# Optimization experiments

Measured on AMD Instinct MI355X. Metric: run time of the kernel, lower is better.

## Reference

```python
import jax, jax.numpy as jnp
import numpy as np

B, P, C = 4, 12000, 64
H, W = 512, 512


def setup_inputs() -> dict:
    key = jax.random.key(0)
    k1, k2 = jax.random.split(key)
    pillar_features = jax.random.normal(k1, (B, P, C), dtype=jnp.float32)
    coords = jax.random.randint(k2, (B, P, 4), 0, 512, dtype=jnp.int32)
    return {"pillar_features": pillar_features, "coords": coords}


def reference(pillar_features, coords):
    # pillar_features: [B, P, C], coords: [B, P, 4] with (batch, y, x, z)
    y_idx = coords[:, :, 1].astype(jnp.int32)  # [B, P]
    x_idx = coords[:, :, 2].astype(jnp.int32)  # [B, P]
    valid = (x_idx >= 0) & (x_idx < W) & (y_idx >= 0) & (y_idx < H)
    # Route invalid points out of bounds; mode='drop' discards them.
    y_safe = jnp.where(valid, y_idx, H)
    x_safe = jnp.where(valid, x_idx, W)
    b_idx = jnp.broadcast_to(jnp.arange(B, dtype=jnp.int32)[:, None], (B, P))
    # Scatter into channels-last canvas, then transpose to [B, C, H, W].
    canvas = jnp.zeros((B, H, W, C), dtype=pillar_features.dtype)
    canvas = canvas.at[b_idx, y_safe, x_safe].set(pillar_features, mode="drop")
    return jnp.transpose(canvas, (0, 3, 1, 2))
```

## Files before the change

kernel.cpp:

```cpp
#include <hip/hip_runtime.h>

#define BB 4
#define PP 12000
#define CC 64
#define HH 512
#define WW 512

__global__ void __launch_bounds__(256) winner_scatter(
    const int* __restrict__ coords, int* __restrict__ winner) {
    int tid = blockIdx.x * blockDim.x + threadIdx.x;
    if (tid >= BB * PP) return;
    int4 c4 = ((const int4*)coords)[tid];
    int y = c4.y;
    int x = c4.z;
    if (x >= 0 && x < WW && y >= 0 && y < HH) {
        int b = tid / PP;
        int p = tid - b * PP;
        atomicMax(&winner[(b * HH + y) * WW + x], p);
    }
}

__global__ void __launch_bounds__(256) fill_out(
    const float* __restrict__ feat, const int* __restrict__ winner,
    float* __restrict__ out) {
    int tid = blockIdx.x * blockDim.x + threadIdx.x;
    int x4   = tid & (WW / 4 - 1);
    int rest = tid >> 7;
    int y = rest & (HH - 1);
    int b = rest >> 9;

    int cell = (b * HH + y) * WW + x4 * 4;
    int4 w4 = *(const int4*)(winner + cell);

    const float* fbase = feat + (size_t)b * PP * CC;
    float* obase = out + ((size_t)(b * CC) * HH + y) * WW + x4 * 4;

#pragma unroll 8
    for (int c = 0; c < CC; ++c) {
        float4 v;
        v.x = (w4.x >= 0) ? fbase[(size_t)w4.x * CC + c] : 0.0f;
        v.y = (w4.y >= 0) ? fbase[(size_t)w4.y * CC + c] : 0.0f;
        v.z = (w4.z >= 0) ? fbase[(size_t)w4.z * CC + c] : 0.0f;
        v.w = (w4.w >= 0) ? fbase[(size_t)w4.w * CC + c] : 0.0f;
        *(float4*)(obase + (size_t)c * HH * WW) = v;
    }
}

extern "C" void kernel_launch(void* const* d_in, const int* in_sizes, int n_in,
                              void* d_out, int out_size, void* d_ws, size_t ws_size,
                              hipStream_t stream) {
    const float* feat  = (const float*)d_in[0];
    const int*   coords = (const int*)d_in[1];
    float* out = (float*)d_out;
    int* winner = (int*)d_ws;

    hipMemsetAsync(winner, 0xFF, (size_t)BB * HH * WW * sizeof(int), stream);

    {
        int n = BB * PP;
        winner_scatter<<<(n + 255) / 256, 256, 0, stream>>>(coords, winner);
    }

    {
        int n = BB * HH * WW / 4;
        fill_out<<<(n + 255) / 256, 256, 0, stream>>>(feat, winner, out);
    }
}
```

Before: 280.5 us.

## Parallelize fill over channels with one float4 per thread and nontemporal stores

The fill kernel now launches one thread per output float4 across all channels, where before each thread looped over the 64 channels. Stores become fully linear over the output and use nontemporal hints so the large write-only canvas does not pollute cache. The cost is that each thread rereads the winner int4, 64 times more often in total, and feature gathers are no longer reused within a thread.

```diff
diff --git a/kernel.cpp b/kernel.cpp
--- a/kernel.cpp
+++ b/kernel.cpp
@@ -20,36 +20,33 @@
     }
 }
 
-__global__ void __launch_bounds__(256) fill_out(
-    const float* __restrict__ feat, const int* __restrict__ winner,
-    float* __restrict__ out) {
+typedef float f4_ev __attribute__((ext_vector_type(4)));
+
+__global__ void __launch_bounds__(256) fill_linear(
+    const float* __restrict__ feat, const int4* __restrict__ winner4,
+    float4* __restrict__ out4) {
     int tid = blockIdx.x * blockDim.x + threadIdx.x;
-    int x4   = tid & (WW / 4 - 1);
-    int rest = tid >> 7;
-    int y = rest & (HH - 1);
-    int b = rest >> 9;
+    int x4 = tid & (WW / 4 - 1);
+    int y  = (tid >> 7) & (HH - 1);
+    int c  = (tid >> 16) & (CC - 1);
+    int b  = tid >> 22;
 
-    int cell = (b * HH + y) * WW + x4 * 4;
-    int4 w4 = *(const int4*)(winner + cell);
+    int4 w4 = winner4[(b * HH + y) * (WW / 4) + x4];
 
-    const float* fbase = feat + (size_t)b * PP * CC;
-    float* obase = out + ((size_t)(b * CC) * HH + y) * WW + x4 * 4;
+    const float* fbase = feat + (size_t)b * (PP * CC) + c;
+    float4 v;
+    v.x = (w4.x >= 0) ? fbase[(size_t)w4.x * CC] : 0.0f;
+    v.y = (w4.y >= 0) ? fbase[(size_t)w4.y * CC] : 0.0f;
+    v.z = (w4.z >= 0) ? fbase[(size_t)w4.z * CC] : 0.0f;
+    v.w = (w4.w >= 0) ? fbase[(size_t)w4.w * CC] : 0.0f;
 
-#pragma unroll 8
-    for (int c = 0; c < CC; ++c) {
-        float4 v;
-        v.x = (w4.x >= 0) ? fbase[(size_t)w4.x * CC + c] : 0.0f;
-        v.y = (w4.y >= 0) ? fbase[(size_t)w4.y * CC + c] : 0.0f;
-        v.z = (w4.z >= 0) ? fbase[(size_t)w4.z * CC + c] : 0.0f;
-        v.w = (w4.w >= 0) ? fbase[(size_t)w4.w * CC + c] : 0.0f;
-        *(float4*)(obase + (size_t)c * HH * WW) = v;
-    }
+    __builtin_nontemporal_store(*(const f4_ev*)&v, (f4_ev*)&out4[tid]);
 }
 
 extern "C" void kernel_launch(void* const* d_in, const int* in_sizes, int n_in,
                               void* d_out, int out_size, void* d_ws, size_t ws_size,
                               hipStream_t stream) {
-    const float* feat  = (const float*)d_in[0];
+    const float* feat   = (const float*)d_in[0];
     const int*   coords = (const int*)d_in[1];
     float* out = (float*)d_out;
     int* winner = (int*)d_ws;
@@ -62,7 +59,8 @@
     }
 
     {
-        int n = BB * HH * WW / 4;
-        fill_out<<<(n + 255) / 256, 256, 0, stream>>>(feat, winner, out);
+        int n = BB * CC * HH * WW / 4;
+        fill_linear<<<n / 256, 256, 0, stream>>>(
+            feat, (const int4*)winner, (float4*)out);
     }
 }
```

New measurement: 277.7 us. About the same (-1.0%).
